# Performance work log

Measured on AMD Instinct MI355X. Metric: run time of the kernel, lower is better.

Reference implementation:

```python
import jax, jax.numpy as jnp
from jax import lax
import numpy as np

B, C, H, W, HID = 16, 8, 512, 512, 16


def setup_inputs() -> dict:
    key = jax.random.key(0)
    k1, k2, k3, k4, k5 = jax.random.split(key, 5)
    x = jax.random.normal(k1, (B, C, H, W), dtype=jnp.float32)
    w1_w = jax.random.normal(k2, (HID, 4 * C), dtype=jnp.float32) * 0.1  # 1x1 conv 32->16
    w1_b = jax.random.normal(k3, (HID,), dtype=jnp.float32) * 0.1
    w2_w = jax.random.normal(k4, (C, HID), dtype=jnp.float32) * 0.1     # 1x1 conv 16->8, no bias
    update_mask = jax.random.randint(k5, (B, 1, H, W), 0, 2, dtype=jnp.int32)  # floor(rand+0.5)
    return {"x": x, "w1_w": w1_w, "w1_b": w1_b, "w2_w": w2_w, "update_mask": update_mask}


def _fixed_filters(dtype):
    ident = jnp.zeros((3, 3), dtype).at[1, 1].set(1.0)
    sobel_x = jnp.array([[-1.0, 0.0, 1.0], [-2.0, 0.0, 2.0], [-1.0, 0.0, 1.0]], dtype) / 8.0
    lap = jnp.array([[1.0, 2.0, 1.0], [2.0, -12.0, 2.0], [1.0, 2.0, 1.0]], dtype) / 16.0
    return jnp.stack([ident, sobel_x, sobel_x.T, lap])  # [4,3,3]


def _perception(x):
    b, c, h, w = x.shape
    filt = _fixed_filters(x.dtype)
    xp = jnp.pad(x, ((0, 0), (0, 0), (1, 1), (1, 1)), mode="wrap")  # circular pad
    y = lax.conv_general_dilated(
        xp.reshape(b * c, 1, h + 2, w + 2), filt[:, None], (1, 1), "VALID",
        dimension_numbers=("NCHW", "OIHW", "NCHW"))  # [b*c,4,h,w]
    return y.reshape(b, c * 4, h, w)  # channel-major: (c0f0..c0f3, c1f0.., ...)


def reference(x, w1_w, w1_b, w2_w, update_mask):
    dt = 1.0
    y = _perception(x)                                   # [B,4C,H,W]
    y = jax.nn.relu(jnp.einsum("bchw,oc->bohw", y, w1_w) + w1_b[None, :, None, None])
    y = jnp.einsum("bchw,oc->bohw", y, w2_w)             # [B,C,H,W]
    return x + dt * y * update_mask.astype(x.dtype)
```

## Files before the change

kernel.cpp:

```cpp
#include <hip/hip_runtime.h>
#include <hip/hip_bf16.h>
#include <stdint.h>


constexpr int B = 16, C = 8, H = 512, W = 512, HID = 16;
constexpr int HW = H * W;

constexpr int ROWF = 520;
constexpr int CHF  = 4 * ROWF + 8;
constexpr int LDSF = 8 * CHF;

typedef __attribute__((ext_vector_type(8))) short bf16x8;
typedef __attribute__((ext_vector_type(4))) float f32x4;
typedef const __attribute__((address_space(1))) void* as1cp;
typedef __attribute__((address_space(3))) void* as3p;

__device__ __host__ inline uint32_t bf16rne(float f) {
    const uint32_t u = __float_as_uint(f);
    return (u + 0x7fffu + ((u >> 16) & 1u)) >> 16;
}
__device__ inline float bf16tof(uint32_t hs) { return __uint_as_float(hs << 16); }

__device__ inline uint32_t pk2(float a, float b) {
    union { __hip_bfloat162 h; uint32_t u; } r;
    r.h = __float22bfloat162_rn(make_float2(a, b));
    return r.u;
}

__global__ void repack(const float* __restrict__ w1w,
                       const float* __restrict__ w1b,
                       const float* __restrict__ w2w,
                       float* __restrict__ wdf) {
    uint32_t* wd = (uint32_t*)wdf;
    const int t = threadIdx.x;
    if (t >= 64) return;
    const int h = t & 15, kg = t >> 4;
    uint32_t whi[4] = {0, 0, 0, 0}, wlo[4] = {0, 0, 0, 0}, w2f[4] = {0, 0, 0, 0};
    for (int j = 0; j < 8; ++j) {
        const int k = kg * 8 + j, ch = k >> 2, f = k & 3;
        const float* wr = w1w + h * 32 + ch * 4;
        const float we = (f == 0) ? (wr[0] - wr[3])
                       : (f == 3) ? wr[3] * 0.0625f
                                  : wr[f] * 0.125f;
        const uint32_t hs = bf16rne(we);
        const uint32_t ls = bf16rne(we - bf16tof(hs));
        whi[j >> 1] |= hs << (16 * (j & 1));
        wlo[j >> 1] |= ls << (16 * (j & 1));
    }
    for (int j = 0; j < 4; ++j) {
        const float v = (h < 8) ? w2w[h * 16 + kg * 4 + j] : 0.0f;
        w2f[j >> 1] |= bf16rne(v) << (16 * (j & 1));
    }
    for (int q = 0; q < 4; ++q) {
        wd[t * 4 + q]       = whi[q];
        wd[256 + t * 4 + q] = wlo[q];
        wd[512 + t * 4 + q] = w2f[q];
    }
    if (t < 16) wdf[768 + t] = w1b[t];
}

__global__ __launch_bounds__(512, 4) void nca_step_kernel(
    const float* __restrict__ x,
    const int*   __restrict__ mask,
    float*       __restrict__ out,
    const float* __restrict__ wdf)
{
    __shared__ float S[LDSF];

    const int bid = blockIdx.x;
    const int l   = (bid & 7) * 512 + (bid >> 3);
    const int b   = l >> 8;
    const int y0  = (l & 255) << 1;

    const int tid  = threadIdx.x;
    const int lane = tid & 63;
    const int wv   = tid >> 6;

    const float* xb = x + (size_t)b * C * HW;
    const int*   mb = mask + (size_t)b * HW;

    const int rel = wv >> 2;
    const int y   = y0 + rel;
    const int grp = lane >> 4;
    const int p   = lane & 15;
    const int chA = grp * 2;

    int msk[8];
#pragma unroll
    for (int i = 0; i < 8; ++i)
        msk[i] = mb[y * W + ((wv & 3) + 4 * i) * 16 + p];

    union { uint4 u; bf16x8 v; } whiU, wloU, w2U;
    whiU.u = ((const uint4*)wdf)[lane];
    wloU.u = ((const uint4*)wdf)[64 + lane];
    w2U.u  = ((const uint4*)wdf)[128 + lane];
    const f32x4 bias4 = ((const f32x4*)(wdf + 768))[lane >> 4];

    {
        const int rs   = (wv >> 1) & 3;
        const int hf   = wv & 1;
        const int grow = (y0 - 1 + rs) & (H - 1);
        const int goff = grow * W + hf * 256 + lane * 4;
        const int loff = rs * ROWF + 4 + hf * 256;
#pragma unroll
        for (int ch = 0; ch < 8; ++ch) {
            const float* src = xb + ch * HW + goff;
            float* dst = S + ch * CHF + loff;
            __builtin_amdgcn_global_load_lds((as1cp)src, (as3p)dst, 16, 0, 0);
        }
    }
    __syncthreads();
    if (tid < 64) {
        const int r = tid >> 1;
        float* rb = S + (r >> 2) * CHF + (r & 3) * ROWF;
        if (tid & 1) rb[516] = rb[4];
        else         rb[3]   = rb[515];
    }
    __syncthreads();

    float* ob = out + (size_t)b * C * HW;

#pragma unroll
    for (int i = 0; i < 8; ++i) {
        const int g  = (wv & 3) + i * 4;
        const int px = g * 16 + p;
        const int ci = px + 3;

        float f_[8];
#pragma unroll
        for (int cc = 0; cc < 2; ++cc) {
            const float* R0 = S + (chA + cc) * CHF + rel * ROWF + ci;
            const float* R1 = R0 + ROWF;
            const float* R2 = R1 + ROWF;
            const float a0 = R0[0], a1 = R0[1], a2 = R0[2];
            const float b0 = R1[0], b1 = R1[1], b2 = R1[2];
            const float c0 = R2[0], c1 = R2[1], c2 = R2[2];
            const float s0 = fmaf(2.f, b0, a0 + c0);
            const float s1 = fmaf(2.f, b1, a1 + c1);
            const float s2 = fmaf(2.f, b2, a2 + c2);
            const float d0 = c0 - a0, d1 = c1 - a1, d2 = c2 - a2;
            f_[cc * 4 + 0] = b1;
            f_[cc * 4 + 1] = s2 - s0;
            f_[cc * 4 + 2] = fmaf(2.f, d1, d0 + d2);
            f_[cc * 4 + 3] = fmaf(2.f, s1, s0 + s2);
        }

        union { uint32_t u[4]; bf16x8 v; } bh = {{
            pk2(f_[0], f_[1]), pk2(f_[2], f_[3]),
            pk2(f_[4], f_[5]), pk2(f_[6], f_[7])}};

        f32x4 acc = bias4;
        acc = __builtin_amdgcn_mfma_f32_16x16x32_bf16(whiU.v, bh.v, acc, 0, 0, 0);
        acc = __builtin_amdgcn_mfma_f32_16x16x32_bf16(wloU.v, bh.v, acc, 0, 0, 0);

        union { uint32_t u[4]; bf16x8 v; } b2 = {{
            pk2(fmaxf(acc[0], 0.f), fmaxf(acc[1], 0.f)),
            pk2(fmaxf(acc[2], 0.f), fmaxf(acc[3], 0.f)), 0, 0}};
        f32x4 d2 = {0.f, 0.f, 0.f, 0.f};
        d2 = __builtin_amdgcn_mfma_f32_16x16x32_bf16(w2U.v, b2.v, d2, 0, 0, 0);

        if (lane < 32) {
            const float mfv = (float)msk[i];
            const int och0 = grp * 4;
            float* op = ob + y * W + px;
#pragma unroll
            for (int r = 0; r < 4; ++r) {
                const float xv =
                    S[(och0 + r) * CHF + (rel + 1) * ROWF + 4 + px];
                op[(och0 + r) * HW] = fmaf(d2[r], mfv, xv);
            }
        }
    }
}

extern "C" void kernel_launch(void* const* d_in, const int* in_sizes, int n_in,
                              void* d_out, int out_size, void* d_ws, size_t ws_size,
                              hipStream_t stream) {
    const float* x    = (const float*)d_in[0];
    const float* w1w  = (const float*)d_in[1];
    const float* w1b  = (const float*)d_in[2];
    const float* w2w  = (const float*)d_in[3];
    const int*   mask = (const int*)d_in[4];
    float* out = (float*)d_out;
    float* wdf = (float*)d_ws;

    hipLaunchKernelGGL(repack, dim3(1), dim3(64), 0, stream,
                       w1w, w1b, w2w, wdf);
    hipLaunchKernelGGL(nca_step_kernel, dim3(B * H / 2), dim3(512), 0, stream,
                       x, mask, out, wdf);
}
```

Baseline: 83.60 us.

## Store the input tile in LDS as packed bf16 to halve shared memory

The staged 3-row by 8-channel halo tile is now converted to bf16 in registers and stored packed in LDS, replacing direct global-to-LDS fp32 loads. Stencil taps are unpacked from 32-bit word pairs with parity-based selection. The launch-bounds occupancy hint is raised from 4 to 8 blocks. This roughly halves the LDS footprint so more blocks can be resident to hide memory latency. In exchange, loads go through registers, and the residual x added to the output is now taken from bf16, which reduces output accuracy.

```diff
diff --git a/kernel.cpp b/kernel.cpp
--- a/kernel.cpp
+++ b/kernel.cpp
@@ -6,14 +6,12 @@
 constexpr int B = 16, C = 8, H = 512, W = 512, HID = 16;
 constexpr int HW = H * W;
 
-constexpr int ROWF = 520;
-constexpr int CHF  = 4 * ROWF + 8;
-constexpr int LDSF = 8 * CHF;
+constexpr int ROWU = 264;
+constexpr int CHB  = 4 * ROWU + 8;
+constexpr int LDSU = 8 * CHB;
 
 typedef __attribute__((ext_vector_type(8))) short bf16x8;
 typedef __attribute__((ext_vector_type(4))) float f32x4;
-typedef const __attribute__((address_space(1))) void* as1cp;
-typedef __attribute__((address_space(3))) void* as3p;
 
 __device__ __host__ inline uint32_t bf16rne(float f) {
     const uint32_t u = __float_as_uint(f);
@@ -59,13 +57,14 @@
     if (t < 16) wdf[768 + t] = w1b[t];
 }
 
-__global__ __launch_bounds__(512, 4) void nca_step_kernel(
+__global__ __launch_bounds__(512, 8) void nca_step_kernel(
     const float* __restrict__ x,
     const int*   __restrict__ mask,
     float*       __restrict__ out,
     const float* __restrict__ wdf)
 {
-    __shared__ float S[LDSF];
+    __shared__ uint32_t S32[LDSU];
+    uint16_t* Sh = (uint16_t*)S32;
 
     const int bid = blockIdx.x;
     const int l   = (bid & 7) * 512 + (bid >> 3);
@@ -85,56 +84,85 @@
     const int p   = lane & 15;
     const int chA = grp * 2;
 
-    int msk[8];
-#pragma unroll
-    for (int i = 0; i < 8; ++i)
-        msk[i] = mb[y * W + ((wv & 3) + 4 * i) * 16 + p];
+    {
+        const int rs   = (wv >> 1) & 3;
+        const int hf   = wv & 1;
+        const int grow = (y0 - 1 + rs) & (H - 1);
+        const int gbase = grow * W + hf * 256 + lane * 4;
+        const int lbase = rs * ROWU + 2 + hf * 128 + lane * 2;
+        const float4 v0 = *(const float4*)(xb + 0 * HW + gbase);
+        const float4 v1 = *(const float4*)(xb + 1 * HW + gbase);
+        const float4 v2 = *(const float4*)(xb + 2 * HW + gbase);
+        const float4 v3 = *(const float4*)(xb + 3 * HW + gbase);
+        S32[0 * CHB + lbase] = pk2(v0.x, v0.y);
+        S32[0 * CHB + lbase + 1] = pk2(v0.z, v0.w);
+        S32[1 * CHB + lbase] = pk2(v1.x, v1.y);
+        S32[1 * CHB + lbase + 1] = pk2(v1.z, v1.w);
+        S32[2 * CHB + lbase] = pk2(v2.x, v2.y);
+        S32[2 * CHB + lbase + 1] = pk2(v2.z, v2.w);
+        S32[3 * CHB + lbase] = pk2(v3.x, v3.y);
+        S32[3 * CHB + lbase + 1] = pk2(v3.z, v3.w);
+        const float4 v4 = *(const float4*)(xb + 4 * HW + gbase);
+        const float4 v5 = *(const float4*)(xb + 5 * HW + gbase);
+        const float4 v6 = *(const float4*)(xb + 6 * HW + gbase);
+        const float4 v7 = *(const float4*)(xb + 7 * HW + gbase);
+        S32[4 * CHB + lbase] = pk2(v4.x, v4.y);
+        S32[4 * CHB + lbase + 1] = pk2(v4.z, v4.w);
+        S32[5 * CHB + lbase] = pk2(v5.x, v5.y);
+        S32[5 * CHB + lbase + 1] = pk2(v5.z, v5.w);
+        S32[6 * CHB + lbase] = pk2(v6.x, v6.y);
+        S32[6 * CHB + lbase + 1] = pk2(v6.z, v6.w);
+        S32[7 * CHB + lbase] = pk2(v7.x, v7.y);
+        S32[7 * CHB + lbase + 1] = pk2(v7.z, v7.w);
+    }
 
     union { uint4 u; bf16x8 v; } whiU, wloU, w2U;
     whiU.u = ((const uint4*)wdf)[lane];
     wloU.u = ((const uint4*)wdf)[64 + lane];
     w2U.u  = ((const uint4*)wdf)[128 + lane];
     const f32x4 bias4 = ((const f32x4*)(wdf + 768))[lane >> 4];
-
-    {
-        const int rs   = (wv >> 1) & 3;
-        const int hf   = wv & 1;
-        const int grow = (y0 - 1 + rs) & (H - 1);
-        const int goff = grow * W + hf * 256 + lane * 4;
-        const int loff = rs * ROWF + 4 + hf * 256;
-#pragma unroll
-        for (int ch = 0; ch < 8; ++ch) {
-            const float* src = xb + ch * HW + goff;
-            float* dst = S + ch * CHF + loff;
-            __builtin_amdgcn_global_load_lds((as1cp)src, (as3p)dst, 16, 0, 0);
-        }
-    }
+    int msk[8];
+#pragma unroll
+    for (int i = 0; i < 8; ++i)
+        msk[i] = mb[y * W + ((wv & 3) + 4 * i) * 16 + p];
+
     __syncthreads();
     if (tid < 64) {
         const int r = tid >> 1;
-        float* rb = S + (r >> 2) * CHF + (r & 3) * ROWF;
+        uint16_t* rb = Sh + ((r >> 2) * CHB + (r & 3) * ROWU) * 2;
         if (tid & 1) rb[516] = rb[4];
         else         rb[3]   = rb[515];
     }
     __syncthreads();
 
     float* ob = out + (size_t)b * C * HW;
+
+    const bool ev = (p & 1) != 0;
+
+#define EXT3(aa0, aa1, aa2, ux, uy) do {                                   \
+    const uint32_t xl_ = (ux) << 16, xh_ = (ux) & 0xFFFF0000u;             \
+    const uint32_t yl_ = (uy) << 16, yh_ = (uy) & 0xFFFF0000u;             \
+    aa0 = __uint_as_float(ev ? xl_ : xh_);                                 \
+    aa1 = __uint_as_float(ev ? xh_ : yl_);                                 \
+    aa2 = __uint_as_float(ev ? yl_ : yh_); } while (0)
 
 #pragma unroll
     for (int i = 0; i < 8; ++i) {
         const int g  = (wv & 3) + i * 4;
         const int px = g * 16 + p;
-        const int ci = px + 3;
+        const int eu = (px + 3) >> 1;
 
         float f_[8];
 #pragma unroll
         for (int cc = 0; cc < 2; ++cc) {
-            const float* R0 = S + (chA + cc) * CHF + rel * ROWF + ci;
-            const float* R1 = R0 + ROWF;
-            const float* R2 = R1 + ROWF;
-            const float a0 = R0[0], a1 = R0[1], a2 = R0[2];
-            const float b0 = R1[0], b1 = R1[1], b2 = R1[2];
-            const float c0 = R2[0], c1 = R2[1], c2 = R2[2];
+            const uint32_t* Rc = S32 + (chA + cc) * CHB + rel * ROWU + eu;
+            const uint32_t ux0 = Rc[0],            uy0 = Rc[1];
+            const uint32_t ux1 = Rc[ROWU],         uy1 = Rc[ROWU + 1];
+            const uint32_t ux2 = Rc[2 * ROWU],     uy2 = Rc[2 * ROWU + 1];
+            float a0, a1, a2, b0, b1, b2, c0, c1, c2;
+            EXT3(a0, a1, a2, ux0, uy0);
+            EXT3(b0, b1, b2, ux1, uy1);
+            EXT3(c0, c1, c2, ux2, uy2);
             const float s0 = fmaf(2.f, b0, a0 + c0);
             const float s1 = fmaf(2.f, b1, a1 + c1);
             const float s2 = fmaf(2.f, b2, a2 + c2);
@@ -165,12 +193,14 @@
             float* op = ob + y * W + px;
 #pragma unroll
             for (int r = 0; r < 4; ++r) {
-                const float xv =
-                    S[(och0 + r) * CHF + (rel + 1) * ROWF + 4 + px];
+                const uint32_t xr =
+                    Sh[((och0 + r) * CHB + (rel + 1) * ROWU) * 2 + px + 4];
+                const float xv = __uint_as_float(xr << 16);
                 op[(och0 + r) * HW] = fmaf(d2[r], mfv, xv);
             }
         }
     }
+#undef EXT3
 }
 
 extern "C" void kernel_launch(void* const* d_in, const int* in_sizes, int n_in,
```

Measured after the change: 86.54 us. 3.5% more time.

## Fold stencil filters into bf16 MFMA weights and stage packed bf16 tiles in LDS

Applied to the files above, without the earlier changes.

The fixed perception filters are folded into three row-wise weight matrices on the host-side repack, so the main kernel feeds bf16 neighbour pairs straight from LDS into six MFMAs per tile instead of computing Sobel and Laplacian values with VALU work. The x halo rows are loaded with regular vector loads, converted to bf16 pairs (even and odd shifted copies) and stored in LDS. The mask is staged into LDS with async global-to-LDS loads instead of per-lane register loads. The residual x term is now read back from bf16 LDS data, which adds rounding error to the output and may break accuracy. The kernel also does three times more MFMA work and more conversion ALU work.

```diff
diff --git a/kernel.cpp b/kernel.cpp
--- a/kernel.cpp
+++ b/kernel.cpp
@@ -6,9 +6,11 @@
 constexpr int B = 16, C = 8, H = 512, W = 512, HID = 16;
 constexpr int HW = H * W;
 
-constexpr int ROWF = 520;
-constexpr int CHF  = 4 * ROWF + 8;
-constexpr int LDSF = 8 * CHF;
+constexpr int ROW32 = 520;
+constexpr int CH32  = 4 * ROW32 + 8;
+constexpr int XTOT  = 8 * CH32;
+constexpr int MOFF  = XTOT;
+constexpr int LDSU  = XTOT + 2 * 512;
 
 typedef __attribute__((ext_vector_type(8))) short bf16x8;
 typedef __attribute__((ext_vector_type(4))) float f32x4;
@@ -19,8 +21,9 @@
     const uint32_t u = __float_as_uint(f);
     return (u + 0x7fffu + ((u >> 16) & 1u)) >> 16;
 }
-__device__ inline float bf16tof(uint32_t hs) { return __uint_as_float(hs << 16); }
-
+__device__ __host__ inline float bf16tof(uint32_t hs) {
+    union { uint32_t u; float f; } c; c.u = hs << 16; return c.f;
+}
 __device__ inline uint32_t pk2(float a, float b) {
     union { __hip_bfloat162 h; uint32_t u; } r;
     r.h = __float22bfloat162_rn(make_float2(a, b));
@@ -35,28 +38,40 @@
     const int t = threadIdx.x;
     if (t >= 64) return;
     const int h = t & 15, kg = t >> 4;
-    uint32_t whi[4] = {0, 0, 0, 0}, wlo[4] = {0, 0, 0, 0}, w2f[4] = {0, 0, 0, 0};
-    for (int j = 0; j < 8; ++j) {
-        const int k = kg * 8 + j, ch = k >> 2, f = k & 3;
-        const float* wr = w1w + h * 32 + ch * 4;
-        const float we = (f == 0) ? (wr[0] - wr[3])
-                       : (f == 3) ? wr[3] * 0.0625f
-                                  : wr[f] * 0.125f;
-        const uint32_t hs = bf16rne(we);
-        const uint32_t ls = bf16rne(we - bf16tof(hs));
-        whi[j >> 1] |= hs << (16 * (j & 1));
-        wlo[j >> 1] |= ls << (16 * (j & 1));
-    }
+    const float SX[3][3] = {{-0.125f, 0.f, 0.125f},
+                            {-0.25f,  0.f, 0.25f},
+                            {-0.125f, 0.f, 0.125f}};
+    const float LP[3][3] = {{0.0625f, 0.125f, 0.0625f},
+                            {0.125f, -0.75f,  0.125f},
+                            {0.0625f, 0.125f, 0.0625f}};
+    for (int q = 0; q < 3; ++q) {
+        uint32_t whi[4] = {0, 0, 0, 0}, wlo[4] = {0, 0, 0, 0};
+        for (int j = 0; j < 8; ++j) {
+            const int ch = 2 * kg + (j >> 2), slot = j & 3;
+            float w = 0.0f;
+            if (slot < 3) {
+                const float* wr = w1w + h * 32 + ch * 4;
+                const int iy = q, ix = slot;
+                w = wr[1] * SX[iy][ix] + wr[2] * SX[ix][iy] + wr[3] * LP[iy][ix];
+                if (q == 1 && slot == 1) w += wr[0];
+            }
+            const uint32_t hs = bf16rne(w);
+            const uint32_t ls = bf16rne(w - bf16tof(hs));
+            whi[j >> 1] |= hs << (16 * (j & 1));
+            wlo[j >> 1] |= ls << (16 * (j & 1));
+        }
+        for (int qq = 0; qq < 4; ++qq) {
+            wd[q * 512 + t * 4 + qq]       = whi[qq];
+            wd[q * 512 + 256 + t * 4 + qq] = wlo[qq];
+        }
+    }
+    uint32_t w2f[4] = {0, 0, 0, 0};
     for (int j = 0; j < 4; ++j) {
         const float v = (h < 8) ? w2w[h * 16 + kg * 4 + j] : 0.0f;
         w2f[j >> 1] |= bf16rne(v) << (16 * (j & 1));
     }
-    for (int q = 0; q < 4; ++q) {
-        wd[t * 4 + q]       = whi[q];
-        wd[256 + t * 4 + q] = wlo[q];
-        wd[512 + t * 4 + q] = w2f[q];
-    }
-    if (t < 16) wdf[768 + t] = w1b[t];
+    for (int qq = 0; qq < 4; ++qq) wd[1536 + t * 4 + qq] = w2f[qq];
+    if (t < 16) wdf[1792 + t] = w1b[t];
 }
 
 __global__ __launch_bounds__(512, 4) void nca_step_kernel(
@@ -65,7 +80,7 @@
     float*       __restrict__ out,
     const float* __restrict__ wdf)
 {
-    __shared__ float S[LDSF];
+    __shared__ uint32_t S32[LDSU];
 
     const int bid = blockIdx.x;
     const int l   = (bid & 7) * 512 + (bid >> 3);
@@ -78,80 +93,84 @@
 
     const float* xb = x + (size_t)b * C * HW;
     const int*   mb = mask + (size_t)b * HW;
+
+#pragma unroll
+    for (int k = 0; k < 8; ++k) {
+        const int c     = tid + 512 * k;
+        const int rowch = c >> 7;
+        const int m4    = c & 127;
+        const int ch    = rowch >> 2, rs = rowch & 3;
+        const int grow  = (y0 - 1 + rs) & (H - 1);
+        const float* xr = xb + ch * HW + grow * W;
+        const float4 v  = *(const float4*)(xr + 4 * m4);
+        const float  x4 = xr[(4 * m4 + 4) & (W - 1)];
+        uint32_t* rbase = S32 + ch * CH32 + rs * ROW32;
+        *(uint2*)(rbase + 2 * m4)       = make_uint2(pk2(v.x, v.y), pk2(v.z, v.w));
+        *(uint2*)(rbase + 260 + 2 * m4) = make_uint2(pk2(v.y, v.z), pk2(v.w, x4));
+    }
+    if (tid < 64) {
+        const int rowch = tid >> 1;
+        const int ch = rowch >> 2, rs = rowch & 3;
+        const int grow = (y0 - 1 + rs) & (H - 1);
+        const float* xr = xb + ch * HW + grow * W;
+        uint32_t* rbase = S32 + ch * CH32 + rs * ROW32;
+        if (tid & 1) rbase[256] = pk2(xr[0], xr[1]);
+        else         rbase[259] = pk2(xr[511], xr[0]);
+    }
+    if (wv < 4) {
+        const int mr = wv >> 1, hf = wv & 1;
+        const int* msrc = mb + (y0 + mr) * W + hf * 256 + lane * 4;
+        uint32_t* mdst = S32 + MOFF + mr * 512 + hf * 256;
+        __builtin_amdgcn_global_load_lds((as1cp)msrc, (as3p)mdst, 16, 0, 0);
+    }
+
+    union { uint4 u; bf16x8 v; } wh0, wl0, wh1, wl1, wh2, wl2, w2U;
+    wh0.u = ((const uint4*)wdf)[lane];
+    wl0.u = ((const uint4*)wdf)[64 + lane];
+    wh1.u = ((const uint4*)wdf)[128 + lane];
+    wl1.u = ((const uint4*)wdf)[192 + lane];
+    wh2.u = ((const uint4*)wdf)[256 + lane];
+    wl2.u = ((const uint4*)wdf)[320 + lane];
+    w2U.u = ((const uint4*)wdf)[384 + lane];
+    const f32x4 bias4 = ((const f32x4*)(wdf + 1792))[lane >> 4];
+
+    __syncthreads();
 
     const int rel = wv >> 2;
     const int y   = y0 + rel;
     const int grp = lane >> 4;
     const int p   = lane & 15;
     const int chA = grp * 2;
-
-    int msk[8];
-#pragma unroll
-    for (int i = 0; i < 8; ++i)
-        msk[i] = mb[y * W + ((wv & 3) + 4 * i) * 16 + p];
-
-    union { uint4 u; bf16x8 v; } whiU, wloU, w2U;
-    whiU.u = ((const uint4*)wdf)[lane];
-    wloU.u = ((const uint4*)wdf)[64 + lane];
-    w2U.u  = ((const uint4*)wdf)[128 + lane];
-    const f32x4 bias4 = ((const f32x4*)(wdf + 768))[lane >> 4];
-
-    {
-        const int rs   = (wv >> 1) & 3;
-        const int hf   = wv & 1;
-        const int grow = (y0 - 1 + rs) & (H - 1);
-        const int goff = grow * W + hf * 256 + lane * 4;
-        const int loff = rs * ROWF + 4 + hf * 256;
-#pragma unroll
-        for (int ch = 0; ch < 8; ++ch) {
-            const float* src = xb + ch * HW + goff;
-            float* dst = S + ch * CHF + loff;
-            __builtin_amdgcn_global_load_lds((as1cp)src, (as3p)dst, 16, 0, 0);
-        }
-    }
-    __syncthreads();
-    if (tid < 64) {
-        const int r = tid >> 1;
-        float* rb = S + (r >> 2) * CHF + (r & 3) * ROWF;
-        if (tid & 1) rb[516] = rb[4];
-        else         rb[3]   = rb[515];
-    }
-    __syncthreads();
-
+    const bool podd = (p & 1) != 0;
+    const int px0 = (wv & 3) * 16 + p;
+    const int e1 = podd ? ((px0 - 1) >> 1) : (259 + (px0 >> 1));
+    const int e2 = podd ? ((px0 + 1) >> 1) : (260 + (px0 >> 1));
     float* ob = out + (size_t)b * C * HW;
 
 #pragma unroll
     for (int i = 0; i < 8; ++i) {
-        const int g  = (wv & 3) + i * 4;
-        const int px = g * 16 + p;
-        const int ci = px + 3;
-
-        float f_[8];
-#pragma unroll
-        for (int cc = 0; cc < 2; ++cc) {
-            const float* R0 = S + (chA + cc) * CHF + rel * ROWF + ci;
-            const float* R1 = R0 + ROWF;
-            const float* R2 = R1 + ROWF;
-            const float a0 = R0[0], a1 = R0[1], a2 = R0[2];
-            const float b0 = R1[0], b1 = R1[1], b2 = R1[2];
-            const float c0 = R2[0], c1 = R2[1], c2 = R2[2];
-            const float s0 = fmaf(2.f, b0, a0 + c0);
-            const float s1 = fmaf(2.f, b1, a1 + c1);
-            const float s2 = fmaf(2.f, b2, a2 + c2);
-            const float d0 = c0 - a0, d1 = c1 - a1, d2 = c2 - a2;
-            f_[cc * 4 + 0] = b1;
-            f_[cc * 4 + 1] = s2 - s0;
-            f_[cc * 4 + 2] = fmaf(2.f, d1, d0 + d2);
-            f_[cc * 4 + 3] = fmaf(2.f, s1, s0 + s2);
-        }
-
-        union { uint32_t u[4]; bf16x8 v; } bh = {{
-            pk2(f_[0], f_[1]), pk2(f_[2], f_[3]),
-            pk2(f_[4], f_[5]), pk2(f_[6], f_[7])}};
+        const int px = px0 + 64 * i;
+        const int o32 = 32 * i;
+
+        const uint32_t* bA = S32 + chA * CH32 + rel * ROW32;
+        const uint32_t* bB = bA + CH32;
+        union { uint32_t u[4]; bf16x8 v; } f0 = {{
+            bA[e1 + o32],             bA[e2 + o32],
+            bB[e1 + o32],             bB[e2 + o32]}};
+        union { uint32_t u[4]; bf16x8 v; } f1 = {{
+            bA[ROW32 + e1 + o32],     bA[ROW32 + e2 + o32],
+            bB[ROW32 + e1 + o32],     bB[ROW32 + e2 + o32]}};
+        union { uint32_t u[4]; bf16x8 v; } f2 = {{
+            bA[2 * ROW32 + e1 + o32], bA[2 * ROW32 + e2 + o32],
+            bB[2 * ROW32 + e1 + o32], bB[2 * ROW32 + e2 + o32]}};
 
         f32x4 acc = bias4;
-        acc = __builtin_amdgcn_mfma_f32_16x16x32_bf16(whiU.v, bh.v, acc, 0, 0, 0);
-        acc = __builtin_amdgcn_mfma_f32_16x16x32_bf16(wloU.v, bh.v, acc, 0, 0, 0);
+        acc = __builtin_amdgcn_mfma_f32_16x16x32_bf16(wh0.v, f0.v, acc, 0, 0, 0);
+        acc = __builtin_amdgcn_mfma_f32_16x16x32_bf16(wl0.v, f0.v, acc, 0, 0, 0);
+        acc = __builtin_amdgcn_mfma_f32_16x16x32_bf16(wh1.v, f1.v, acc, 0, 0, 0);
+        acc = __builtin_amdgcn_mfma_f32_16x16x32_bf16(wl1.v, f1.v, acc, 0, 0, 0);
+        acc = __builtin_amdgcn_mfma_f32_16x16x32_bf16(wh2.v, f2.v, acc, 0, 0, 0);
+        acc = __builtin_amdgcn_mfma_f32_16x16x32_bf16(wl2.v, f2.v, acc, 0, 0, 0);
 
         union { uint32_t u[4]; bf16x8 v; } b2 = {{
             pk2(fmaxf(acc[0], 0.f), fmaxf(acc[1], 0.f)),
@@ -160,13 +179,16 @@
         d2 = __builtin_amdgcn_mfma_f32_16x16x32_bf16(w2U.v, b2.v, d2, 0, 0, 0);
 
         if (lane < 32) {
-            const float mfv = (float)msk[i];
+            const float mfv =
+                (float)((const int*)(S32 + MOFF))[rel * 512 + px];
             const int och0 = grp * 4;
             float* op = ob + y * W + px;
 #pragma unroll
             for (int r = 0; r < 4; ++r) {
-                const float xv =
-                    S[(och0 + r) * CHF + (rel + 1) * ROWF + 4 + px];
+                const uint32_t vv =
+                    S32[(och0 + r) * CH32 + (rel + 1) * ROW32 + (px >> 1)];
+                const float xv = __uint_as_float(podd ? (vv & 0xffff0000u)
+                                                      : (vv << 16));
                 op[(och0 + r) * HW] = fmaf(d2[r], mfv, xv);
             }
         }
```

After: 89.08 us. +6.6%, slower.
